# Kernel optimization log

Measured on AMD Instinct MI355X. Metric: run time of the kernel, lower is better.

## Reference

```python
import jax, jax.numpy as jnp
import numpy as np

# --- module hyperparameters (match init_kwargs) ---
B, CIN, COUT, K = 32, 2, 2, 16
FEAT_DIM = 256
FRAME_SIZE, OVERLAP = 160, 40
NUM_FRAMES = 500
NUM_SAMPLES = NUM_FRAMES * FRAME_SIZE
FFT_SIZE = 512  # 2**ceil(log2(2*frame_size + overlap))
SHAPE_GAIN_DB = -6.0
GAIN_LIMITS_DB = (-6.0, 6.0)
LN10_DIV_20 = 0.11512925464970229


def setup_inputs() -> dict:
    key = jax.random.key(0)
    ks = jax.random.split(key, 6)
    x = jax.random.normal(ks[0], (B, CIN, NUM_SAMPLES), dtype=jnp.float32)
    features = jax.random.normal(ks[1], (B, NUM_FRAMES, FEAT_DIM), dtype=jnp.float32)
    # nn.Linear(feature_dim, in*out*K) and nn.Linear(feature_dim, out) params
    conv_kernel_w = jax.random.normal(ks[2], (COUT * CIN * K, FEAT_DIM), jnp.float32) / np.float32(np.sqrt(FEAT_DIM))
    conv_kernel_b = jax.random.normal(ks[3], (COUT * CIN * K,), jnp.float32) * 0.01
    filter_gain_w = jax.random.normal(ks[4], (COUT, FEAT_DIM), jnp.float32) / np.float32(np.sqrt(FEAT_DIM))
    filter_gain_b = jax.random.normal(ks[5], (COUT,), jnp.float32) * 0.01
    # fixed raised-cosine fade-out window (requires_grad=False buffer)
    n = jnp.arange(OVERLAP, dtype=jnp.float32)
    overlap_win = 0.5 + 0.5 * jnp.cos((n + 0.5) * jnp.pi / OVERLAP)
    return {"x": x, "features": features,
            "conv_kernel_w": conv_kernel_w, "conv_kernel_b": conv_kernel_b,
            "filter_gain_w": filter_gain_w, "filter_gain_b": filter_gain_b,
            "overlap_win": overlap_win}


def _forward(x, features, ck_w, ck_b, fg_w, fg_b, overlap_win):
    B_, F_, _ = features.shape
    log_min = GAIN_LIMITS_DB[0] * LN10_DIV_20
    log_max = GAIN_LIMITS_DB[1] * LN10_DIV_20
    gain_a = (log_max - log_min) / 2.0
    gain_b = (log_max + log_min) / 2.0
    shape_gain = min(1.0, 10.0 ** (SHAPE_GAIN_DB / 20.0))
    id_tap = K - 1 - K // 2  # padding[1]

    # per-frame kernels: (B, F, Cout, Cin, K)
    ck = (features @ ck_w.T + ck_b).reshape(B_, F_, COUT, CIN, K)
    # norm_p = 2 over (Cin, K)
    ck = ck / (1e-6 + jnp.sqrt(jnp.sum(ck * ck, axis=(-2, -1), keepdims=True)))
    idk = jnp.zeros_like(ck).at[..., id_tap].set(1.0)
    ck = shape_gain * ck + (1.0 - shape_gain) * idk
    gains = jnp.exp(gain_a * jnp.tanh(features @ fg_w.T + fg_b) + gain_b)  # (B,F,Cout)
    w = jnp.transpose(ck * gains[..., None, None], (0, 2, 3, 1, 4))  # (B,Cout,Cin,F,K)

    win1 = jnp.flip(overlap_win)  # fade-in (expansion_power == 1)
    win2 = overlap_win            # fade-out (== 1 - win1)

    # frame the input with K-1 lookback and OVERLAP lookahead samples
    xp = jnp.pad(x, ((0, 0), (0, 0), (K - 1, OVERLAP)))
    L = FRAME_SIZE + K - 1 + OVERLAP
    idx = jnp.arange(F_)[:, None] * FRAME_SIZE + jnp.arange(L)[None, :]
    frames = xp[:, :, idx]  # (B, Cin, F, L)

    # FFT convolution, summing over input channels in the frequency domain
    X = jnp.fft.rfft(frames, n=FFT_SIZE)          # (B,Cin,F,nf)
    Wf = jnp.fft.rfft(w, n=FFT_SIZE)              # (B,Cout,Cin,F,nf)
    Yf = jnp.einsum('bifn,boifn->bofn', X, Wf)
    Y = jnp.fft.irfft(Yf, n=FFT_SIZE)[..., K - 1: K - 1 + FRAME_SIZE + OVERLAP]  # (B,Cout,F,fs+ov)

    # windowed overlap-add crossfade between consecutive frame filters
    head = Y[..., :FRAME_SIZE].at[..., :OVERLAP].multiply(win1)
    tail = Y[..., FRAME_SIZE:] * win2  # (B,Cout,F,ov)
    out = head.at[:, :, 1:, :OVERLAP].add(tail[:, :, :-1])
    return out.reshape(B_, COUT, F_ * FRAME_SIZE)


def reference(x, features, conv_kernel_w, conv_kernel_b, filter_gain_w, filter_gain_b, overlap_win):
    return _forward(x, features, conv_kernel_w, conv_kernel_b, filter_gain_w, filter_gain_b, overlap_win)
```

## Files before the change

### kernel.cpp

```cpp
#include <hip/hip_runtime.h>

#define BB    32
#define NF    500
#define FRAME 160
#define OV    40
#define KK    16
#define NS    (NF * FRAME)
#define FEAT  256

#define NBODY2 (BB * NF * 15)
#define NOV2   (BB * NF * 5)

__device__ const float GAIN_A     = 0.6907755278982137f;
__device__ const float SHAPE_GAIN = 0.5011872336272722f;

__global__ __launch_bounds__(512, 4) void wcalc6_kernel(
    const float* __restrict__ feats,
    const float* __restrict__ ckw,
    const float* __restrict__ ckb,
    const float* __restrict__ fgw,
    const float* __restrict__ fgb,
    float* __restrict__ wout)
{
    int tile = blockIdx.x;
    int b    = blockIdx.y;
    int z    = blockIdx.z;
    int f0   = tile * 64;
    int tid  = threadIdx.x;
    int w    = tid >> 6;
    int l    = tid & 63;

    __shared__ float sf[64 * 128];
    __shared__ float sr[8][64];

    int rbase = __builtin_amdgcn_readfirstlane(z * 32 + w * 4);
    const float* gw0 = fgw + z * FEAT;

    float acc[4] = {0.f, 0.f, 0.f, 0.f};
    float g = 0.f;

    for (int h = 0; h < 2; ++h) {
        __syncthreads();
        #pragma unroll
        for (int p = 0; p < 4; ++p) {
            int F  = p * 512 + tid;
            int fr = F >> 5;
            int c4 = F & 31;
            int f  = f0 + fr;
            float4 v = make_float4(0.f, 0.f, 0.f, 0.f);
            if (f < NF)
                v = *(const float4*)(feats + ((size_t)(b * NF + f)) * FEAT
                                     + h * 128 + c4 * 4);
            *(float4*)(sf + fr * 128 + ((c4 ^ (fr & 7)) * 4)) = v;
        }
        __syncthreads();

        #pragma unroll 2
        for (int cl = 0; cl < 16; ++cl) {
            float4 fa = *(const float4*)(sf + l * 128 + (((2 * cl)     ^ (l & 7)) * 4));
            float4 fb = *(const float4*)(sf + l * 128 + (((2 * cl + 1) ^ (l & 7)) * 4));
            float fr8[8] = {fa.x, fa.y, fa.z, fa.w, fb.x, fb.y, fb.z, fb.w};
            int kg = h * 128 + cl * 8;
            #pragma unroll
            for (int r = 0; r < 4; ++r) {
                const float* wp = ckw + (size_t)(rbase + r) * FEAT + kg;
                #pragma unroll
                for (int i = 0; i < 8; ++i)
                    acc[r] = fmaf(fr8[i], wp[i], acc[r]);
            }
            const float* gp = gw0 + kg;
            #pragma unroll
            for (int i = 0; i < 8; ++i)
                g = fmaf(fr8[i], gp[i], g);
        }
    }

    #pragma unroll
    for (int r = 0; r < 4; ++r) acc[r] += ckb[rbase + r];
    g += fgb[z];

    float ssq = 0.f;
    #pragma unroll
    for (int r = 0; r < 4; ++r) ssq = fmaf(acc[r], acc[r], ssq);
    sr[w][l] = ssq;
    __syncthreads();
    float tot = 0.f;
    #pragma unroll
    for (int j = 0; j < 8; ++j) tot += sr[j][l];
    float norm = 1e-6f + sqrtf(tot);

    float gain = expf(GAIN_A * tanhf(g));
    float sc   = gain * SHAPE_GAIN / norm;
    float idv  = gain * (1.0f - SHAPE_GAIN);

    int f = f0 + l;
    if (f < NF) {
        float o[4];
        #pragma unroll
        for (int r = 0; r < 4; ++r)
            o[r] = acc[r] * sc + ((((rbase + r) & 15) == 7) ? idv : 0.f);
        float4 v;
        v.x = o[0]; v.y = o[1]; v.z = o[2]; v.w = o[3];
        *(float4*)(wout + ((size_t)(b * NF + f)) * 64 + rbase) = v;
    }
}

__global__ __launch_bounds__(256) void conv2_kernel(
    const float* __restrict__ x,
    const float* __restrict__ w,
    const float* __restrict__ owin,
    float* __restrict__ out)
{
    int flat = blockIdx.x * 256 + threadIdx.x;
    if (flat < NBODY2) {
        int g    = flat % 15;
        int rest = flat / 15;
        int f    = rest % NF;
        int b    = rest / NF;
        int s0   = f * FRAME + OV + g * 8;

        const float* xb = x + (size_t)b * 2 * NS;
        float xr[2][24];
        #pragma unroll
        for (int ci = 0; ci < 2; ++ci) {
            const float* xc = xb + (size_t)ci * NS + s0 - 16;
            #pragma unroll
            for (int c = 0; c < 6; ++c) {
                float4 v = *(const float4*)(xc + c * 4);
                xr[ci][c * 4 + 0] = v.x; xr[ci][c * 4 + 1] = v.y;
                xr[ci][c * 4 + 2] = v.z; xr[ci][c * 4 + 3] = v.w;
            }
        }
        const float* wfb = w + (size_t)(b * NF + f) * 64;
        #pragma unroll
        for (int cout = 0; cout < 2; ++cout) {
            const float4* wf = (const float4*)(wfb + cout * 32);
            float wr[32];
            #pragma unroll
            for (int q = 0; q < 8; ++q) {
                float4 v = wf[q];
                wr[q * 4 + 0] = v.x; wr[q * 4 + 1] = v.y;
                wr[q * 4 + 2] = v.z; wr[q * 4 + 3] = v.w;
            }
            float acc[8];
            #pragma unroll
            for (int j = 0; j < 8; ++j) acc[j] = 0.f;
            #pragma unroll
            for (int ci = 0; ci < 2; ++ci)
                #pragma unroll
                for (int k = 0; k < KK; ++k) {
                    float wk = wr[ci * 16 + k];
                    #pragma unroll
                    for (int j = 0; j < 8; ++j)
                        acc[j] = fmaf(wk, xr[ci][16 + j - k], acc[j]);
                }
            float* dst = out + (size_t)(b * 2 + cout) * NS + s0;
            float4 v0, v1;
            v0.x = acc[0]; v0.y = acc[1]; v0.z = acc[2]; v0.w = acc[3];
            v1.x = acc[4]; v1.y = acc[5]; v1.z = acc[6]; v1.w = acc[7];
            *(float4*)(dst)     = v0;
            *(float4*)(dst + 4) = v1;
        }
    } else {
        int flat2 = flat - NBODY2;
        int g    = flat2 % 5;
        int rest = flat2 / 5;
        int f    = rest % NF;
        int b    = rest / NF;
        int t0   = g * 8;
        int s0   = f * FRAME + t0;

        const float* xb = x + (size_t)b * 2 * NS;
        float xr[2][24];
        #pragma unroll
        for (int ci = 0; ci < 2; ++ci) {
            const float* xc = xb + (size_t)ci * NS + s0 - 16;
            #pragma unroll
            for (int c = 0; c < 6; ++c) {
                if (s0 - 16 + c * 4 >= 0) {
                    float4 v = *(const float4*)(xc + c * 4);
                    xr[ci][c * 4 + 0] = v.x; xr[ci][c * 4 + 1] = v.y;
                    xr[ci][c * 4 + 2] = v.z; xr[ci][c * 4 + 3] = v.w;
                } else {
                    xr[ci][c * 4 + 0] = 0.f; xr[ci][c * 4 + 1] = 0.f;
                    xr[ci][c * 4 + 2] = 0.f; xr[ci][c * 4 + 3] = 0.f;
                }
            }
        }

        float o_tail[8], o_head[8];
        {
            float4 a = *(const float4*)(owin + t0);
            float4 c = *(const float4*)(owin + t0 + 4);
            o_tail[0] = a.x; o_tail[1] = a.y; o_tail[2] = a.z; o_tail[3] = a.w;
            o_tail[4] = c.x; o_tail[5] = c.y; o_tail[6] = c.z; o_tail[7] = c.w;
            float4 d = *(const float4*)(owin + (32 - t0));
            float4 e = *(const float4*)(owin + (36 - t0));
            o_head[0] = e.w; o_head[1] = e.z; o_head[2] = e.y; o_head[3] = e.x;
            o_head[4] = d.w; o_head[5] = d.z; o_head[6] = d.y; o_head[7] = d.x;
        }

        const float* wfb = w + (size_t)(b * NF + f) * 64;
        #pragma unroll
        for (int cout = 0; cout < 2; ++cout) {
            float res[8];
            #pragma unroll
            for (int j = 0; j < 8; ++j) res[j] = 0.f;

            float wr[32];
            if (f > 0) {
                const float4* wp = (const float4*)(wfb - 64 + cout * 32);
                #pragma unroll
                for (int q = 0; q < 8; ++q) {
                    float4 v = wp[q];
                    wr[q * 4 + 0] = v.x; wr[q * 4 + 1] = v.y;
                    wr[q * 4 + 2] = v.z; wr[q * 4 + 3] = v.w;
                }
                float acc[8];
                #pragma unroll
                for (int j = 0; j < 8; ++j) acc[j] = 0.f;
                #pragma unroll
                for (int ci = 0; ci < 2; ++ci)
                    #pragma unroll
                    for (int k = 0; k < KK; ++k) {
                        float wk = wr[ci * 16 + k];
                        #pragma unroll
                        for (int j = 0; j < 8; ++j)
                            acc[j] = fmaf(wk, xr[ci][16 + j - k], acc[j]);
                    }
                #pragma unroll
                for (int j = 0; j < 8; ++j) res[j] = o_tail[j] * acc[j];
            }
            {
                const float4* wf = (const float4*)(wfb + cout * 32);
                #pragma unroll
                for (int q = 0; q < 8; ++q) {
                    float4 v = wf[q];
                    wr[q * 4 + 0] = v.x; wr[q * 4 + 1] = v.y;
                    wr[q * 4 + 2] = v.z; wr[q * 4 + 3] = v.w;
                }
                float acc[8];
                #pragma unroll
                for (int j = 0; j < 8; ++j) acc[j] = 0.f;
                #pragma unroll
                for (int ci = 0; ci < 2; ++ci)
                    #pragma unroll
                    for (int k = 0; k < KK; ++k) {
                        float wk = wr[ci * 16 + k];
                        #pragma unroll
                        for (int j = 0; j < 8; ++j)
                            acc[j] = fmaf(wk, xr[ci][16 + j - k], acc[j]);
                    }
                #pragma unroll
                for (int j = 0; j < 8; ++j)
                    res[j] = fmaf(o_head[j], acc[j], res[j]);
            }
            float* dst = out + (size_t)(b * 2 + cout) * NS + s0;
            float4 v0, v1;
            v0.x = res[0]; v0.y = res[1]; v0.z = res[2]; v0.w = res[3];
            v1.x = res[4]; v1.y = res[5]; v1.z = res[6]; v1.w = res[7];
            *(float4*)(dst)     = v0;
            *(float4*)(dst + 4) = v1;
        }
    }
}

extern "C" void kernel_launch(void* const* d_in, const int* in_sizes, int n_in,
                              void* d_out, int out_size, void* d_ws, size_t ws_size,
                              hipStream_t stream) {
    const float* x     = (const float*)d_in[0];
    const float* feats = (const float*)d_in[1];
    const float* ckw   = (const float*)d_in[2];
    const float* ckb   = (const float*)d_in[3];
    const float* fgw   = (const float*)d_in[4];
    const float* fgb   = (const float*)d_in[5];
    const float* owin  = (const float*)d_in[6];
    float* out  = (float*)d_out;
    float* wbuf = (float*)d_ws;

    hipLaunchKernelGGL(wcalc6_kernel, dim3(8, BB, 2), dim3(512), 0, stream,
                       feats, ckw, ckb, fgw, fgb, wbuf);

    hipLaunchKernelGGL(conv2_kernel, dim3((NBODY2 + NOV2) / 256), dim3(256), 0, stream,
                       x, wbuf, owin, out);
}
```

Before: 119.6 us.

## Stage input and filter taps in LDS per 12-frame chunk for conv

```diff
diff --git a/kernel.cpp b/kernel.cpp
--- a/kernel.cpp
+++ b/kernel.cpp
@@ -8,8 +8,8 @@
 #define NS    (NF * FRAME)
 #define FEAT  256
 
-#define NBODY2 (BB * NF * 15)
-#define NOV2   (BB * NF * 5)
+#define CHUNK  12
+#define NCHUNK 42
 
 __device__ const float GAIN_A     = 0.6907755278982137f;
 __device__ const float SHAPE_GAIN = 0.5011872336272722f;
@@ -105,163 +105,121 @@
     }
 }
 
-__global__ __launch_bounds__(256) void conv2_kernel(
+__global__ __launch_bounds__(256, 4) void conv3_kernel(
     const float* __restrict__ x,
     const float* __restrict__ w,
     const float* __restrict__ owin,
     float* __restrict__ out)
 {
-    int flat = blockIdx.x * 256 + threadIdx.x;
-    if (flat < NBODY2) {
-        int g    = flat % 15;
-        int rest = flat / 15;
-        int f    = rest % NF;
-        int b    = rest / NF;
-        int s0   = f * FRAME + OV + g * 8;
-
-        const float* xb = x + (size_t)b * 2 * NS;
-        float xr[2][24];
-        #pragma unroll
-        for (int ci = 0; ci < 2; ++ci) {
-            const float* xc = xb + (size_t)ci * NS + s0 - 16;
-            #pragma unroll
-            for (int c = 0; c < 6; ++c) {
-                float4 v = *(const float4*)(xc + c * 4);
-                xr[ci][c * 4 + 0] = v.x; xr[ci][c * 4 + 1] = v.y;
-                xr[ci][c * 4 + 2] = v.z; xr[ci][c * 4 + 3] = v.w;
-            }
-        }
-        const float* wfb = w + (size_t)(b * NF + f) * 64;
-        #pragma unroll
-        for (int cout = 0; cout < 2; ++cout) {
-            const float4* wf = (const float4*)(wfb + cout * 32);
-            float wr[32];
-            #pragma unroll
-            for (int q = 0; q < 8; ++q) {
-                float4 v = wf[q];
-                wr[q * 4 + 0] = v.x; wr[q * 4 + 1] = v.y;
-                wr[q * 4 + 2] = v.z; wr[q * 4 + 3] = v.w;
-            }
-            float acc[8];
-            #pragma unroll
-            for (int j = 0; j < 8; ++j) acc[j] = 0.f;
-            #pragma unroll
-            for (int ci = 0; ci < 2; ++ci)
-                #pragma unroll
-                for (int k = 0; k < KK; ++k) {
-                    float wk = wr[ci * 16 + k];
-                    #pragma unroll
-                    for (int j = 0; j < 8; ++j)
-                        acc[j] = fmaf(wk, xr[ci][16 + j - k], acc[j]);
+    int chunk = blockIdx.x;
+    int b     = blockIdx.y;
+    int c0    = chunk * CHUNK;
+    int tid   = threadIdx.x;
+
+    __shared__ float sx[2 * 1936];
+    __shared__ float sw[13 * 64];
+    __shared__ float so[40];
+
+    const float* xb = x + (size_t)b * 2 * NS;
+    int s_base = c0 * FRAME - 16;
+    #pragma unroll
+    for (int p = 0; p < 4; ++p) {
+        int idx = p * 256 + tid;
+        if (idx < 968) {
+            int ci = idx / 484;
+            int q  = idx - ci * 484;
+            int g  = s_base + q * 4;
+            float4 v;
+            if (g >= 0 && g + 4 <= NS) {
+                v = *(const float4*)(xb + (size_t)ci * NS + g);
+            } else {
+                float t[4];
+                #pragma unroll
+                for (int e = 0; e < 4; ++e) {
+                    int gg = g + e;
+                    t[e] = (gg >= 0 && gg < NS) ? xb[(size_t)ci * NS + gg] : 0.f;
                 }
-            float* dst = out + (size_t)(b * 2 + cout) * NS + s0;
-            float4 v0, v1;
-            v0.x = acc[0]; v0.y = acc[1]; v0.z = acc[2]; v0.w = acc[3];
-            v1.x = acc[4]; v1.y = acc[5]; v1.z = acc[6]; v1.w = acc[7];
-            *(float4*)(dst)     = v0;
-            *(float4*)(dst + 4) = v1;
-        }
-    } else {
-        int flat2 = flat - NBODY2;
-        int g    = flat2 % 5;
-        int rest = flat2 / 5;
-        int f    = rest % NF;
-        int b    = rest / NF;
-        int t0   = g * 8;
-        int s0   = f * FRAME + t0;
-
-        const float* xb = x + (size_t)b * 2 * NS;
-        float xr[2][24];
-        #pragma unroll
-        for (int ci = 0; ci < 2; ++ci) {
-            const float* xc = xb + (size_t)ci * NS + s0 - 16;
-            #pragma unroll
-            for (int c = 0; c < 6; ++c) {
-                if (s0 - 16 + c * 4 >= 0) {
-                    float4 v = *(const float4*)(xc + c * 4);
-                    xr[ci][c * 4 + 0] = v.x; xr[ci][c * 4 + 1] = v.y;
-                    xr[ci][c * 4 + 2] = v.z; xr[ci][c * 4 + 3] = v.w;
-                } else {
-                    xr[ci][c * 4 + 0] = 0.f; xr[ci][c * 4 + 1] = 0.f;
-                    xr[ci][c * 4 + 2] = 0.f; xr[ci][c * 4 + 3] = 0.f;
-                }
-            }
-        }
-
-        float o_tail[8], o_head[8];
-        {
-            float4 a = *(const float4*)(owin + t0);
-            float4 c = *(const float4*)(owin + t0 + 4);
-            o_tail[0] = a.x; o_tail[1] = a.y; o_tail[2] = a.z; o_tail[3] = a.w;
-            o_tail[4] = c.x; o_tail[5] = c.y; o_tail[6] = c.z; o_tail[7] = c.w;
-            float4 d = *(const float4*)(owin + (32 - t0));
-            float4 e = *(const float4*)(owin + (36 - t0));
-            o_head[0] = e.w; o_head[1] = e.z; o_head[2] = e.y; o_head[3] = e.x;
-            o_head[4] = d.w; o_head[5] = d.z; o_head[6] = d.y; o_head[7] = d.x;
-        }
-
-        const float* wfb = w + (size_t)(b * NF + f) * 64;
-        #pragma unroll
-        for (int cout = 0; cout < 2; ++cout) {
-            float res[8];
-            #pragma unroll
-            for (int j = 0; j < 8; ++j) res[j] = 0.f;
-
-            float wr[32];
+                v = make_float4(t[0], t[1], t[2], t[3]);
+            }
+            *(float4*)(sx + ci * 1936 + q * 4) = v;
+        }
+    }
+    if (tid < 208) {
+        int r  = tid >> 4;
+        int c4 = tid & 15;
+        int f  = c0 - 1 + r;
+        float4 v = make_float4(0.f, 0.f, 0.f, 0.f);
+        if (f >= 0 && f < NF)
+            v = *(const float4*)(w + ((size_t)(b * NF + f)) * 64 + c4 * 4);
+        *(float4*)(sw + r * 64 + c4 * 4) = v;
+    }
+    if (tid < 40) so[tid] = owin[tid];
+    __syncthreads();
+
+    if (tid >= 240) return;
+    int fl = tid / 20;
+    int tt = tid - fl * 20;
+    int f  = c0 + fl;
+    if (f >= NF) return;
+
+    int base = fl * FRAME + tt * 8;
+    int t0   = tt * 8;
+
+    float xw[2][23];
+    #pragma unroll
+    for (int ci = 0; ci < 2; ++ci)
+        #pragma unroll
+        for (int m = 0; m < 23; ++m)
+            xw[ci][m] = sx[ci * 1936 + base + 1 + m];
+
+    const float* wc = sw + (fl + 1) * 64;
+    const float* wp = sw + fl * 64;
+
+    #pragma unroll
+    for (int cout = 0; cout < 2; ++cout) {
+        float acc[8];
+        #pragma unroll
+        for (int j = 0; j < 8; ++j) acc[j] = 0.f;
+        #pragma unroll
+        for (int ci = 0; ci < 2; ++ci)
+            #pragma unroll
+            for (int k = 0; k < KK; ++k) {
+                float wk = wc[cout * 32 + ci * 16 + k];
+                #pragma unroll
+                for (int j = 0; j < 8; ++j)
+                    acc[j] = fmaf(wk, xw[ci][j - k + 15], acc[j]);
+            }
+
+        float res[8];
+        if (t0 < OV) {
+            float accp[8];
+            #pragma unroll
+            for (int j = 0; j < 8; ++j) accp[j] = 0.f;
             if (f > 0) {
-                const float4* wp = (const float4*)(wfb - 64 + cout * 32);
-                #pragma unroll
-                for (int q = 0; q < 8; ++q) {
-                    float4 v = wp[q];
-                    wr[q * 4 + 0] = v.x; wr[q * 4 + 1] = v.y;
-                    wr[q * 4 + 2] = v.z; wr[q * 4 + 3] = v.w;
-                }
-                float acc[8];
-                #pragma unroll
-                for (int j = 0; j < 8; ++j) acc[j] = 0.f;
                 #pragma unroll
                 for (int ci = 0; ci < 2; ++ci)
                     #pragma unroll
                     for (int k = 0; k < KK; ++k) {
-                        float wk = wr[ci * 16 + k];
+                        float wk = wp[cout * 32 + ci * 16 + k];
                         #pragma unroll
                         for (int j = 0; j < 8; ++j)
-                            acc[j] = fmaf(wk, xr[ci][16 + j - k], acc[j]);
+                            accp[j] = fmaf(wk, xw[ci][j - k + 15], accp[j]);
                     }
-                #pragma unroll
-                for (int j = 0; j < 8; ++j) res[j] = o_tail[j] * acc[j];
-            }
-            {
-                const float4* wf = (const float4*)(wfb + cout * 32);
-                #pragma unroll
-                for (int q = 0; q < 8; ++q) {
-                    float4 v = wf[q];
-                    wr[q * 4 + 0] = v.x; wr[q * 4 + 1] = v.y;
-                    wr[q * 4 + 2] = v.z; wr[q * 4 + 3] = v.w;
-                }
-                float acc[8];
-                #pragma unroll
-                for (int j = 0; j < 8; ++j) acc[j] = 0.f;
-                #pragma unroll
-                for (int ci = 0; ci < 2; ++ci)
-                    #pragma unroll
-                    for (int k = 0; k < KK; ++k) {
-                        float wk = wr[ci * 16 + k];
-                        #pragma unroll
-                        for (int j = 0; j < 8; ++j)
-                            acc[j] = fmaf(wk, xr[ci][16 + j - k], acc[j]);
-                    }
-                #pragma unroll
-                for (int j = 0; j < 8; ++j)
-                    res[j] = fmaf(o_head[j], acc[j], res[j]);
-            }
-            float* dst = out + (size_t)(b * 2 + cout) * NS + s0;
-            float4 v0, v1;
-            v0.x = res[0]; v0.y = res[1]; v0.z = res[2]; v0.w = res[3];
-            v1.x = res[4]; v1.y = res[5]; v1.z = res[6]; v1.w = res[7];
-            *(float4*)(dst)     = v0;
-            *(float4*)(dst + 4) = v1;
-        }
+            }
+            #pragma unroll
+            for (int j = 0; j < 8; ++j)
+                res[j] = so[39 - t0 - j] * acc[j] + so[t0 + j] * accp[j];
+        } else {
+            #pragma unroll
+            for (int j = 0; j < 8; ++j) res[j] = acc[j];
+        }
+
+        float* dst = out + (size_t)(b * 2 + cout) * NS + f * FRAME + t0;
+        float4 v0, v1;
+        v0.x = res[0]; v0.y = res[1]; v0.z = res[2]; v0.w = res[3];
+        v1.x = res[4]; v1.y = res[5]; v1.z = res[6]; v1.w = res[7];
+        *(float4*)(dst)     = v0;
+        *(float4*)(dst + 4) = v1;
     }
 }
 
@@ -281,6 +239,6 @@
     hipLaunchKernelGGL(wcalc6_kernel, dim3(8, BB, 2), dim3(512), 0, stream,
                        feats, ckw, ckb, fgw, fgb, wbuf);
 
-    hipLaunchKernelGGL(conv2_kernel, dim3((NBODY2 + NOV2) / 256), dim3(256), 0, stream,
+    hipLaunchKernelGGL(conv3_kernel, dim3(NCHUNK, BB), dim3(256), 0, stream,
                        x, wbuf, owin, out);
 }
```

Measured after the change: 148.1 us. 23.9% more time.
